# Optimization experiments

Measured on AMD Instinct MI355X. Metric: run time of the kernel, lower is better.

## Reference

```python
import jax, jax.numpy as jnp
import numpy as np

B, T, D = 2, 2048, 2048
H, KV, HD = 32, 8, 64
N_REP = H // KV
THETA = 10000.0
NEG_INF = -1e30


def _rope_tables(seq_len, head_dim, theta):
    inv_freq = 1.0 / (theta ** (jnp.arange(0, head_dim, 2, dtype=jnp.float32) / head_dim))
    t = jnp.arange(seq_len, dtype=jnp.float32)
    freqs = jnp.outer(t, inv_freq)                 # (T, HD/2)
    emb = jnp.concatenate([freqs, freqs], axis=-1)  # (T, HD)
    return jnp.cos(emb), jnp.sin(emb)


def _rotate_half(x):
    half = x.shape[-1] // 2
    return jnp.concatenate([-x[..., half:], x[..., :half]], axis=-1)


def setup_inputs() -> dict:
    key = jax.random.key(0)
    ks = jax.random.split(key, 5)
    s = 0.02  # keep logits in a sane range
    x = jax.random.normal(ks[0], (B, T, D), dtype=jnp.float32)
    Wq = jax.random.normal(ks[1], (D, H * HD), dtype=jnp.float32) * s
    Wk = jax.random.normal(ks[2], (D, KV * HD), dtype=jnp.float32) * s
    Wv = jax.random.normal(ks[3], (D, KV * HD), dtype=jnp.float32) * s
    Wo = jax.random.normal(ks[4], (D, D), dtype=jnp.float32) * s
    cos, sin = _rope_tables(T, HD, THETA)  # start_pos=0 since past_kv is None
    return {"x": x, "Wq": Wq, "Wk": Wk, "Wv": Wv, "Wo": Wo, "cos": cos, "sin": sin}


def reference(x, Wq, Wk, Wv, Wo, cos, sin):
    b, t, _ = x.shape
    # projections -> (B, heads, T, HD)
    q = (x @ Wq).reshape(b, t, H, HD).transpose(0, 2, 1, 3)
    k = (x @ Wk).reshape(b, t, KV, HD).transpose(0, 2, 1, 3)
    v = (x @ Wv).reshape(b, t, KV, HD).transpose(0, 2, 1, 3)
    # RoPE (cos/sin broadcast over batch and heads)
    c = cos[None, None, :, :]
    s = sin[None, None, :, :]
    q = q * c + _rotate_half(q) * s
    k = k * c + _rotate_half(k) * s
    # GQA: broadcast KV heads instead of repeat_interleave.
    # repeat_interleave(n_rep, dim=1) maps query head h -> kv head h // n_rep,
    # which equals reshape H -> (KV, N_REP).
    qg = q.reshape(b, KV, N_REP, t, HD)
    scale = 1.0 / jnp.sqrt(jnp.float32(HD))
    scores = jnp.einsum('bgrtd,bgsd->bgrts', qg, k) * scale  # (B,KV,N_REP,T,T)
    causal = jnp.tril(jnp.ones((t, t), dtype=bool))
    scores = jnp.where(causal[None, None, None, :, :], scores, NEG_INF)
    probs = jax.nn.softmax(scores, axis=-1)
    y = jnp.einsum('bgrts,bgsd->bgrtd', probs, v)            # (B,KV,N_REP,T,HD)
    y = y.reshape(b, H, t, HD).transpose(0, 2, 1, 3).reshape(b, t, H * HD)
    return y @ Wo
```

## Files before the change

kernel.cpp:

```cpp
#include <hip/hip_runtime.h>
#include <hip/hip_bf16.h>

constexpr int Bc  = 2;
constexpr int Tc  = 2048;
constexpr int Dc  = 2048;
constexpr int Hc  = 32;
constexpr int KVc = 8;
constexpr int HDc = 64;
constexpr int Mrows = Bc * Tc;
constexpr int QKVW  = 3072;
constexpr float SCALE = 0.125f;

typedef __attribute__((ext_vector_type(8))) short  bf16x8;
typedef __attribute__((ext_vector_type(4))) short  short4v;
typedef __attribute__((ext_vector_type(4))) float  f32x4;

__device__ __forceinline__ short f2bf(float f) {
    unsigned u = __builtin_bit_cast(unsigned, f);
    unsigned r = (u + 0x7FFFu + ((u >> 16) & 1u)) >> 16;
    return (short)(unsigned short)r;
}

__device__ __forceinline__ void load_lds16(const void* g, void* l) {
    __builtin_amdgcn_global_load_lds(
        (const __attribute__((address_space(1))) unsigned int*)g,
        (__attribute__((address_space(3))) unsigned int*)l,
        16, 0, 0);
}

__global__ void conv_bf16(const float* __restrict__ in, short* __restrict__ out, int n) {
    int i = (blockIdx.x * blockDim.x + threadIdx.x) * 8;
    if (i >= n) return;
    f32x4 a = *(const f32x4*)(in + i);
    f32x4 b = *(const f32x4*)(in + i + 4);
    bf16x8 o;
    o[0] = f2bf(a[0]); o[1] = f2bf(a[1]); o[2] = f2bf(a[2]); o[3] = f2bf(a[3]);
    o[4] = f2bf(b[0]); o[5] = f2bf(b[1]); o[6] = f2bf(b[2]); o[7] = f2bf(b[3]);
    *(bf16x8*)(out + i) = o;
}

__global__ __launch_bounds__(256) void transpose_conv(const float* __restrict__ in,
                                                      short* __restrict__ out,
                                                      int N, int ldo, int n0r) {
    __shared__ float T[64][68];
    const int k0 = blockIdx.y * 64;
    const int n0 = blockIdx.x * 64;
    const int t  = threadIdx.x;
    const int c4 = (t & 15) * 4;
    const int rr = t >> 4;
#pragma unroll
    for (int r = 0; r < 4; ++r) {
        int k = rr + 16 * r;
        float4 v = *(const float4*)(in + (size_t)(k0 + k) * N + n0 + c4);
        *(float4*)&T[k][c4] = v;
    }
    __syncthreads();
#pragma unroll
    for (int r = 0; r < 4; ++r) {
        int n = rr + 16 * r;
        short4v s;
        s[0] = f2bf(T[c4 + 0][n]); s[1] = f2bf(T[c4 + 1][n]);
        s[2] = f2bf(T[c4 + 2][n]); s[3] = f2bf(T[c4 + 3][n]);
        *(short4v*)(out + (size_t)(n0r + n0 + n) * ldo + k0 + c4) = s;
    }
}

__global__ __launch_bounds__(256) void gemm_mfma(const short* __restrict__ A,
                                                 const short* __restrict__ Bt,
                                                 float* __restrict__ C,
                                                 int M, int N, int K) {
    __shared__ short Al[128 * 64];
    __shared__ short Bl[128 * 64];
    const int tid = threadIdx.x;
    const int l  = tid & 63;
    const int w  = tid >> 6;
    const int lr = l & 15;
    const int lg = l >> 4;
    const int wm = w >> 1, wn = w & 1;

    const int nwg = gridDim.x * gridDim.y;
    const int bid0 = blockIdx.y * gridDim.x + blockIdx.x;
    const int cpx = nwg >> 3;
    const int swz = (bid0 & 7) * cpx + (bid0 >> 3);
    const int bm = (swz / gridDim.x) * 128;
    const int bn = (swz % gridDim.x) * 128;

    f32x4 acc[4][4];
#pragma unroll
    for (int i = 0; i < 4; ++i)
#pragma unroll
        for (int j = 0; j < 4; ++j) acc[i][j] = f32x4{0.f, 0.f, 0.f, 0.f};

    const int srow_off = l >> 3;
    const int sunit    = l & 7;

    for (int k0 = 0; k0 < K; k0 += 64) {
        __syncthreads();
#pragma unroll
        for (int j = 0; j < 4; ++j) {
            const int q   = w + 4 * j;
            const int row = 8 * q + srow_off;
            const int ug  = sunit ^ (row & 7);
            load_lds16(A  + (size_t)(bm + row) * K + k0 + ug * 8, (short*)Al + 512 * q);
            load_lds16(Bt + (size_t)(bn + row) * K + k0 + ug * 8, (short*)Bl + 512 * q);
        }
        __syncthreads();

#pragma unroll
        for (int ks = 0; ks < 2; ++ks) {
            bf16x8 af[4], bf[4];
#pragma unroll
            for (int mb = 0; mb < 4; ++mb) {
                const int row = wm * 64 + mb * 16 + lr;
                const int u   = (ks * 4 + lg) ^ (row & 7);
                af[mb] = *(const bf16x8*)(Al + row * 64 + u * 8);
            }
#pragma unroll
            for (int nb = 0; nb < 4; ++nb) {
                const int row = wn * 64 + nb * 16 + lr;
                const int u   = (ks * 4 + lg) ^ (row & 7);
                bf[nb] = *(const bf16x8*)(Bl + row * 64 + u * 8);
            }
#pragma unroll
            for (int mb = 0; mb < 4; ++mb)
#pragma unroll
                for (int nb = 0; nb < 4; ++nb)
                    acc[mb][nb] = __builtin_amdgcn_mfma_f32_16x16x32_bf16(
                        af[mb], bf[nb], acc[mb][nb], 0, 0, 0);
        }
    }

#pragma unroll
    for (int mb = 0; mb < 4; ++mb)
#pragma unroll
        for (int r = 0; r < 4; ++r) {
            const int row = bm + wm * 64 + mb * 16 + lg * 4 + r;
            float* cp = C + (size_t)row * N + bn + wn * 64 + lr;
#pragma unroll
            for (int nb = 0; nb < 4; ++nb) cp[nb * 16] = acc[mb][nb][r];
        }
}

__global__ void rope_pack_qk(const float* __restrict__ qkv,
                             const float* __restrict__ cosT,
                             const float* __restrict__ sinT,
                             short* __restrict__ qb, short* __restrict__ kb,
                             int total) {
    int idx = blockIdx.x * blockDim.x + threadIdx.x;
    if (idx >= total) return;
    int d   = idx & 31;
    int hh  = (idx >> 5) % 40;
    int row = idx / (32 * 40);
    int t   = row & (Tc - 1);
    int b   = row >> 11;
    float c = cosT[t * HDc + d];
    float s = sinT[t * HDc + d];
    if (hh < 32) {
        const float* p = qkv + (size_t)row * QKVW + hh * 64;
        float x0 = p[d], x1 = p[d + 32];
        short* qp = qb + (((size_t)(b * Hc + hh) * Tc + t) * 64);
        qp[d]      = f2bf((x0 * c - x1 * s) * SCALE);
        qp[d + 32] = f2bf((x1 * c + x0 * s) * SCALE);
    } else {
        int g = hh - 32;
        const float* p = qkv + (size_t)row * QKVW + 2048 + g * 64;
        float x0 = p[d], x1 = p[d + 32];
        short* kp = kb + (((size_t)(b * KVc + g) * Tc + t) * 64);
        kp[d]      = f2bf(x0 * c - x1 * s);
        kp[d + 32] = f2bf(x1 * c + x0 * s);
    }
}

__global__ __launch_bounds__(256) void pack_vt(const float* __restrict__ qkv,
                                               short* __restrict__ vtb) {
    __shared__ float T[64][68];
    const int t0 = blockIdx.x * 64;
    const int g  = blockIdx.y;
    const int b  = blockIdx.z;
    const int tt = threadIdx.x;
    const int c4 = (tt & 15) * 4;
    const int rr = tt >> 4;
    const float* src = qkv + 2560 + g * 64;
#pragma unroll
    for (int r = 0; r < 4; ++r) {
        int t = rr + 16 * r;
        float4 v = *(const float4*)(src + (size_t)(b * Tc + t0 + t) * QKVW + c4);
        *(float4*)&T[t][c4] = v;
    }
    __syncthreads();
    short* dst = vtb + ((size_t)(b * KVc + g) * 64) * Tc;
#pragma unroll
    for (int r = 0; r < 4; ++r) {
        int d = rr + 16 * r;
        short4v s;
        s[0] = f2bf(T[c4 + 0][d]); s[1] = f2bf(T[c4 + 1][d]);
        s[2] = f2bf(T[c4 + 2][d]); s[3] = f2bf(T[c4 + 3][d]);
        *(short4v*)(dst + (size_t)d * Tc + t0 + c4) = s;
    }
}

__global__ __launch_bounds__(64) void attn_gqa(const short* __restrict__ qb,
                                               const short* __restrict__ kb,
                                               const short* __restrict__ vtb,
                                               short* __restrict__ yb) {
    __shared__ short Ps[16][72];
    const int l  = threadIdx.x;
    const int lr = l & 15;
    const int lg = l >> 4;
    const int h  = blockIdx.y;
    const int b  = blockIdx.z;
    const int g  = h >> 2;

    const short* qhb = qb  + ((size_t)(b * Hc  + h) * Tc) * 64;
    const short* khb = kb  + ((size_t)(b * KVc + g) * Tc) * 64;
    const short* vhb = vtb + ((size_t)(b * KVc + g) * 64) * Tc;

#pragma unroll
    for (int half = 0; half < 2; ++half) {
        const int j   = half ? (127 - (int)blockIdx.x) : (int)blockIdx.x;
        const int qt0 = j * 16;

        bf16x8 qf0 = *(const bf16x8*)(qhb + (size_t)(qt0 + lr) * 64 + lg * 8);
        bf16x8 qf1 = *(const bf16x8*)(qhb + (size_t)(qt0 + lr) * 64 + 32 + lg * 8);

        f32x4 o[4];
#pragma unroll
        for (int i = 0; i < 4; ++i) o[i] = f32x4{0.f, 0.f, 0.f, 0.f};
        float mr[4], ls[4];
#pragma unroll
        for (int i = 0; i < 4; ++i) { mr[i] = -1e30f; ls[i] = 0.f; }

        const int nsteps = (qt0 >> 6) + 1;
        for (int st = 0; st < nsteps; ++st) {
            const int kv0 = st * 64;

            f32x4 c[4];
#pragma unroll
            for (int kbk = 0; kbk < 4; ++kbk) {
                const short* kr = khb + (size_t)(kv0 + 16 * kbk + lr) * 64;
                bf16x8 k0 = *(const bf16x8*)(kr + lg * 8);
                bf16x8 k1 = *(const bf16x8*)(kr + 32 + lg * 8);
                f32x4 acc = f32x4{0.f, 0.f, 0.f, 0.f};
                acc = __builtin_amdgcn_mfma_f32_16x16x32_bf16(qf0, k0, acc, 0, 0, 0);
                acc = __builtin_amdgcn_mfma_f32_16x16x32_bf16(qf1, k1, acc, 0, 0, 0);
                c[kbk] = acc;
            }

            if (st == nsteps - 1) {
#pragma unroll
                for (int kbk = 0; kbk < 4; ++kbk)
#pragma unroll
                    for (int r = 0; r < 4; ++r)
                        if (kv0 + lr + 16 * kbk > qt0 + lg * 4 + r) c[kbk][r] = -1e30f;
            }

#pragma unroll
            for (int r = 0; r < 4; ++r) {
                float tm = fmaxf(fmaxf(c[0][r], c[1][r]), fmaxf(c[2][r], c[3][r]));
                tm = fmaxf(tm, __shfl_xor(tm, 1));
                tm = fmaxf(tm, __shfl_xor(tm, 2));
                tm = fmaxf(tm, __shfl_xor(tm, 4));
                tm = fmaxf(tm, __shfl_xor(tm, 8));
                if (tm > mr[r]) {
                    const float corr = __expf(mr[r] - tm);
                    mr[r] = tm;
                    ls[r] *= corr;
#pragma unroll
                    for (int db = 0; db < 4; ++db) o[db][r] *= corr;
                }
                float rs = 0.f;
#pragma unroll
                for (int kbk = 0; kbk < 4; ++kbk) {
                    float p = __expf(c[kbk][r] - mr[r]);
                    c[kbk][r] = p;
                    rs += p;
                }
                rs += __shfl_xor(rs, 1);
                rs += __shfl_xor(rs, 2);
                rs += __shfl_xor(rs, 4);
                rs += __shfl_xor(rs, 8);
                ls[r] += rs;
#pragma unroll
                for (int kbk = 0; kbk < 4; ++kbk)
                    Ps[lg * 4 + r][lr + 16 * kbk] = f2bf(c[kbk][r]);
            }

#pragma unroll
            for (int ks = 0; ks < 2; ++ks) {
                bf16x8 pa = *(const bf16x8*)&Ps[lr][lg * 8 + ks * 32];
#pragma unroll
                for (int db = 0; db < 4; ++db) {
                    bf16x8 vv = *(const bf16x8*)(vhb + (size_t)(db * 16 + lr) * Tc
                                                 + kv0 + ks * 32 + lg * 8);
                    o[db] = __builtin_amdgcn_mfma_f32_16x16x32_bf16(pa, vv, o[db], 0, 0, 0);
                }
            }
        }

#pragma unroll
        for (int r = 0; r < 4; ++r) {
            const float inv = 1.0f / ls[r];
            short* yp = yb + (size_t)(b * Tc + qt0 + lg * 4 + r) * Dc + h * 64;
#pragma unroll
            for (int db = 0; db < 4; ++db)
                yp[lr + 16 * db] = f2bf(o[db][r] * inv);
        }
    }
}

extern "C" void kernel_launch(void* const* d_in, const int* in_sizes, int n_in,
                              void* d_out, int out_size, void* d_ws, size_t ws_size,
                              hipStream_t stream) {
    const float* x    = (const float*)d_in[0];
    const float* Wq   = (const float*)d_in[1];
    const float* Wk   = (const float*)d_in[2];
    const float* Wv   = (const float*)d_in[3];
    const float* Wo   = (const float*)d_in[4];
    const float* cosT = (const float*)d_in[5];
    const float* sinT = (const float*)d_in[6];
    float* out = (float*)d_out;

    short* xb    = (short*)d_ws;
    short* Wqkvt = xb + (size_t)Mrows * Dc;
    short* Wot   = Wqkvt + (size_t)QKVW * Dc;
    short* ybuf  = Wot + (size_t)Dc * Dc;
    float* qkv   = (float*)(ybuf + (size_t)Mrows * Dc);
    short* qbp = xb;
    short* kbp = Wqkvt;
    short* vtb = Wqkvt + (size_t)Bc * KVc * Tc * 64;

    conv_bf16<<<(Mrows * Dc / 8 + 255) / 256, 256, 0, stream>>>(x, xb, Mrows * Dc);
    transpose_conv<<<dim3(Dc / 64, Dc / 64), 256, 0, stream>>>(Wq, Wqkvt, Dc, Dc, 0);
    transpose_conv<<<dim3(512 / 64, Dc / 64), 256, 0, stream>>>(Wk, Wqkvt, 512, Dc, 2048);
    transpose_conv<<<dim3(512 / 64, Dc / 64), 256, 0, stream>>>(Wv, Wqkvt, 512, Dc, 2560);
    transpose_conv<<<dim3(Dc / 64, Dc / 64), 256, 0, stream>>>(Wo, Wot, Dc, Dc, 0);

    gemm_mfma<<<dim3(QKVW / 128, Mrows / 128), 256, 0, stream>>>(xb, Wqkvt, qkv, Mrows, QKVW, Dc);

    {
        int total = Mrows * (Hc + KVc) * 32;
        rope_pack_qk<<<(total + 255) / 256, 256, 0, stream>>>(qkv, cosT, sinT, qbp, kbp, total);
        pack_vt<<<dim3(Tc / 64, KVc, Bc), 256, 0, stream>>>(qkv, vtb);
    }

    attn_gqa<<<dim3(64, Hc, Bc), 64, 0, stream>>>(qbp, kbp, vtb, ybuf);

    gemm_mfma<<<dim3(Dc / 128, Mrows / 128), 256, 0, stream>>>(ybuf, Wot, out, Mrows, Dc, Dc);
}
```

Measured before the change: 525.3 us.

## Pack four query tiles per attention block and double-buffer K/V register prefetch

The attention kernel now runs four 64-lane waves per block, each owning one consecutive 16-row query tile, instead of one wave handling a balanced pair of tiles. K fragments for the next KV step are prefetched into a second register set, and V fragments are loaded at the start of each step, so global load latency overlaps the QK MFMAs and softmax. This raises register pressure and drops the front/back causal tile pairing, which may worsen load balance across blocks.

```diff
diff --git a/kernel.cpp b/kernel.cpp
--- a/kernel.cpp
+++ b/kernel.cpp
@@ -199,112 +199,138 @@
     }
 }
 
-__global__ __launch_bounds__(64) void attn_gqa(const short* __restrict__ qb,
-                                               const short* __restrict__ kb,
-                                               const short* __restrict__ vtb,
-                                               short* __restrict__ yb) {
-    __shared__ short Ps[16][72];
-    const int l  = threadIdx.x;
+__global__ __launch_bounds__(256, 3) void attn_gqa(const short* __restrict__ qb,
+                                                   const short* __restrict__ kb,
+                                                   const short* __restrict__ vtb,
+                                                   short* __restrict__ yb) {
+    __shared__ short Ps[4][16][72];
+    const int tid = threadIdx.x;
+    const int l  = tid & 63;
+    const int w  = tid >> 6;
     const int lr = l & 15;
     const int lg = l >> 4;
+    const int j  = (blockIdx.x << 2) | w;
     const int h  = blockIdx.y;
     const int b  = blockIdx.z;
     const int g  = h >> 2;
+    const int qt0 = j * 16;
 
     const short* qhb = qb  + ((size_t)(b * Hc  + h) * Tc) * 64;
     const short* khb = kb  + ((size_t)(b * KVc + g) * Tc) * 64;
     const short* vhb = vtb + ((size_t)(b * KVc + g) * 64) * Tc;
 
-#pragma unroll
-    for (int half = 0; half < 2; ++half) {
-        const int j   = half ? (127 - (int)blockIdx.x) : (int)blockIdx.x;
-        const int qt0 = j * 16;
-
-        bf16x8 qf0 = *(const bf16x8*)(qhb + (size_t)(qt0 + lr) * 64 + lg * 8);
-        bf16x8 qf1 = *(const bf16x8*)(qhb + (size_t)(qt0 + lr) * 64 + 32 + lg * 8);
-
-        f32x4 o[4];
-#pragma unroll
-        for (int i = 0; i < 4; ++i) o[i] = f32x4{0.f, 0.f, 0.f, 0.f};
-        float mr[4], ls[4];
-#pragma unroll
-        for (int i = 0; i < 4; ++i) { mr[i] = -1e30f; ls[i] = 0.f; }
-
-        const int nsteps = (qt0 >> 6) + 1;
-        for (int st = 0; st < nsteps; ++st) {
-            const int kv0 = st * 64;
-
-            f32x4 c[4];
+    const bf16x8 qf0 = *(const bf16x8*)(qhb + (size_t)(qt0 + lr) * 64 + lg * 8);
+    const bf16x8 qf1 = *(const bf16x8*)(qhb + (size_t)(qt0 + lr) * 64 + 32 + lg * 8);
+
+    f32x4 o[4];
+#pragma unroll
+    for (int i = 0; i < 4; ++i) o[i] = f32x4{0.f, 0.f, 0.f, 0.f};
+    float mr[4], ls[4];
+#pragma unroll
+    for (int i = 0; i < 4; ++i) { mr[i] = -1e30f; ls[i] = 0.f; }
+
+    const int nsteps = (qt0 >> 6) + 1;
+
+    bf16x8 kfa[8], kfb[8];
+
+#pragma unroll
+    for (int kbk = 0; kbk < 4; ++kbk) {
+        const short* kr = khb + (size_t)(16 * kbk + lr) * 64;
+        kfa[2 * kbk]     = *(const bf16x8*)(kr + lg * 8);
+        kfa[2 * kbk + 1] = *(const bf16x8*)(kr + 32 + lg * 8);
+    }
+
+    auto step = [&](int st, bf16x8 (&kcur)[8], bf16x8 (&knxt)[8]) {
+        const int kv0 = st * 64;
+
+        bf16x8 vv[8];
+#pragma unroll
+        for (int ks = 0; ks < 2; ++ks)
+#pragma unroll
+            for (int db = 0; db < 4; ++db)
+                vv[ks * 4 + db] = *(const bf16x8*)(vhb + (size_t)(db * 16 + lr) * Tc
+                                                   + kv0 + ks * 32 + lg * 8);
+
+        f32x4 c[4];
+#pragma unroll
+        for (int kbk = 0; kbk < 4; ++kbk) {
+            f32x4 acc = f32x4{0.f, 0.f, 0.f, 0.f};
+            acc = __builtin_amdgcn_mfma_f32_16x16x32_bf16(qf0, kcur[2 * kbk],     acc, 0, 0, 0);
+            acc = __builtin_amdgcn_mfma_f32_16x16x32_bf16(qf1, kcur[2 * kbk + 1], acc, 0, 0, 0);
+            c[kbk] = acc;
+        }
+
+        if (st + 1 < nsteps) {
+            const int kn = kv0 + 64;
 #pragma unroll
             for (int kbk = 0; kbk < 4; ++kbk) {
-                const short* kr = khb + (size_t)(kv0 + 16 * kbk + lr) * 64;
-                bf16x8 k0 = *(const bf16x8*)(kr + lg * 8);
-                bf16x8 k1 = *(const bf16x8*)(kr + 32 + lg * 8);
-                f32x4 acc = f32x4{0.f, 0.f, 0.f, 0.f};
-                acc = __builtin_amdgcn_mfma_f32_16x16x32_bf16(qf0, k0, acc, 0, 0, 0);
-                acc = __builtin_amdgcn_mfma_f32_16x16x32_bf16(qf1, k1, acc, 0, 0, 0);
-                c[kbk] = acc;
-            }
-
-            if (st == nsteps - 1) {
-#pragma unroll
-                for (int kbk = 0; kbk < 4; ++kbk)
-#pragma unroll
-                    for (int r = 0; r < 4; ++r)
-                        if (kv0 + lr + 16 * kbk > qt0 + lg * 4 + r) c[kbk][r] = -1e30f;
-            }
-
-#pragma unroll
-            for (int r = 0; r < 4; ++r) {
-                float tm = fmaxf(fmaxf(c[0][r], c[1][r]), fmaxf(c[2][r], c[3][r]));
-                tm = fmaxf(tm, __shfl_xor(tm, 1));
-                tm = fmaxf(tm, __shfl_xor(tm, 2));
-                tm = fmaxf(tm, __shfl_xor(tm, 4));
-                tm = fmaxf(tm, __shfl_xor(tm, 8));
-                if (tm > mr[r]) {
-                    const float corr = __expf(mr[r] - tm);
-                    mr[r] = tm;
-                    ls[r] *= corr;
-#pragma unroll
-                    for (int db = 0; db < 4; ++db) o[db][r] *= corr;
-                }
-                float rs = 0.f;
-#pragma unroll
-                for (int kbk = 0; kbk < 4; ++kbk) {
-                    float p = __expf(c[kbk][r] - mr[r]);
-                    c[kbk][r] = p;
-                    rs += p;
-                }
-                rs += __shfl_xor(rs, 1);
-                rs += __shfl_xor(rs, 2);
-                rs += __shfl_xor(rs, 4);
-                rs += __shfl_xor(rs, 8);
-                ls[r] += rs;
-#pragma unroll
-                for (int kbk = 0; kbk < 4; ++kbk)
-                    Ps[lg * 4 + r][lr + 16 * kbk] = f2bf(c[kbk][r]);
-            }
-
-#pragma unroll
-            for (int ks = 0; ks < 2; ++ks) {
-                bf16x8 pa = *(const bf16x8*)&Ps[lr][lg * 8 + ks * 32];
-#pragma unroll
-                for (int db = 0; db < 4; ++db) {
-                    bf16x8 vv = *(const bf16x8*)(vhb + (size_t)(db * 16 + lr) * Tc
-                                                 + kv0 + ks * 32 + lg * 8);
-                    o[db] = __builtin_amdgcn_mfma_f32_16x16x32_bf16(pa, vv, o[db], 0, 0, 0);
-                }
-            }
+                const short* kr = khb + (size_t)(kn + 16 * kbk + lr) * 64;
+                knxt[2 * kbk]     = *(const bf16x8*)(kr + lg * 8);
+                knxt[2 * kbk + 1] = *(const bf16x8*)(kr + 32 + lg * 8);
+            }
+        }
+
+        if (st == nsteps - 1) {
+#pragma unroll
+            for (int kbk = 0; kbk < 4; ++kbk)
+#pragma unroll
+                for (int r = 0; r < 4; ++r)
+                    if (kv0 + lr + 16 * kbk > qt0 + lg * 4 + r) c[kbk][r] = -1e30f;
         }
 
 #pragma unroll
         for (int r = 0; r < 4; ++r) {
-            const float inv = 1.0f / ls[r];
-            short* yp = yb + (size_t)(b * Tc + qt0 + lg * 4 + r) * Dc + h * 64;
+            float tm = fmaxf(fmaxf(c[0][r], c[1][r]), fmaxf(c[2][r], c[3][r]));
+            tm = fmaxf(tm, __shfl_xor(tm, 1));
+            tm = fmaxf(tm, __shfl_xor(tm, 2));
+            tm = fmaxf(tm, __shfl_xor(tm, 4));
+            tm = fmaxf(tm, __shfl_xor(tm, 8));
+            if (tm > mr[r]) {
+                const float corr = __expf(mr[r] - tm);
+                mr[r] = tm;
+                ls[r] *= corr;
+#pragma unroll
+                for (int db = 0; db < 4; ++db) o[db][r] *= corr;
+            }
+            float rs = 0.f;
+#pragma unroll
+            for (int kbk = 0; kbk < 4; ++kbk) {
+                float p = __expf(c[kbk][r] - mr[r]);
+                c[kbk][r] = p;
+                rs += p;
+            }
+            rs += __shfl_xor(rs, 1);
+            rs += __shfl_xor(rs, 2);
+            rs += __shfl_xor(rs, 4);
+            rs += __shfl_xor(rs, 8);
+            ls[r] += rs;
+#pragma unroll
+            for (int kbk = 0; kbk < 4; ++kbk)
+                Ps[w][lg * 4 + r][lr + 16 * kbk] = f2bf(c[kbk][r]);
+        }
+
+#pragma unroll
+        for (int ks = 0; ks < 2; ++ks) {
+            bf16x8 pa = *(const bf16x8*)&Ps[w][lr][lg * 8 + ks * 32];
 #pragma unroll
             for (int db = 0; db < 4; ++db)
-                yp[lr + 16 * db] = f2bf(o[db][r] * inv);
-        }
+                o[db] = __builtin_amdgcn_mfma_f32_16x16x32_bf16(pa, vv[ks * 4 + db],
+                                                                o[db], 0, 0, 0);
+        }
+    };
+
+    for (int st = 0; st < nsteps; st += 2) {
+        step(st, kfa, kfb);
+        if (st + 1 < nsteps) step(st + 1, kfb, kfa);
+    }
+
+#pragma unroll
+    for (int r = 0; r < 4; ++r) {
+        const float inv = 1.0f / ls[r];
+        short* yp = yb + (size_t)(b * Tc + qt0 + lg * 4 + r) * Dc + h * 64;
+#pragma unroll
+        for (int db = 0; db < 4; ++db)
+            yp[lr + 16 * db] = f2bf(o[db][r] * inv);
     }
 }
 
@@ -343,7 +369,7 @@
         pack_vt<<<dim3(Tc / 64, KVc, Bc), 256, 0, stream>>>(qkv, vtb);
     }
 
-    attn_gqa<<<dim3(64, Hc, Bc), 64, 0, stream>>>(qbp, kbp, vtb, ybuf);
+    attn_gqa<<<dim3(32, Hc, Bc), 256, 0, stream>>>(qbp, kbp, vtb, ybuf);
 
     gemm_mfma<<<dim3(Dc / 128, Mrows / 128), 256, 0, stream>>>(ybuf, Wot, out, Mrows, Dc, Dc);
 }
```

Measured after the change: 757.7 us. +44.2%, slower.

## Process two 16-row query tiles per wave, four waves per attention block

Applied to the files above, without the earlier changes.

The attention kernel now gives each wave a 32-row query tile (two 16-row sub-tiles) and reuses each loaded K fragment and V fragment for both sub-tiles, halving global K/V loads per query row. Blocks grow from one wave to four, with the tiles mixed so that each block's causal work is balanced, and the grid shrinks accordingly. Each wave keeps a private LDS probability buffer guarded by wave-level barriers. In exchange, register pressure rises and the causal mask covers coarser 32-row tiles, so a few extra fully masked key entries get processed.

```diff
diff --git a/kernel.cpp b/kernel.cpp
--- a/kernel.cpp
+++ b/kernel.cpp
@@ -26,6 +26,12 @@
         (const __attribute__((address_space(1))) unsigned int*)g,
         (__attribute__((address_space(3))) unsigned int*)l,
         16, 0, 0);
+}
+
+__device__ __forceinline__ void lds_fence() {
+    __builtin_amdgcn_sched_barrier(0);
+    __builtin_amdgcn_wave_barrier();
+    __builtin_amdgcn_sched_barrier(0);
 }
 
 __global__ void conv_bf16(const float* __restrict__ in, short* __restrict__ out, int n) {
@@ -199,111 +205,145 @@
     }
 }
 
-__global__ __launch_bounds__(64) void attn_gqa(const short* __restrict__ qb,
-                                               const short* __restrict__ kb,
-                                               const short* __restrict__ vtb,
-                                               short* __restrict__ yb) {
-    __shared__ short Ps[16][72];
-    const int l  = threadIdx.x;
+__global__ __launch_bounds__(256, 2) void attn_gqa(const short* __restrict__ qb,
+                                                   const short* __restrict__ kb,
+                                                   const short* __restrict__ vtb,
+                                                   short* __restrict__ yb) {
+    __shared__ short Ps[4][2][16][72];
+    const int tid = threadIdx.x;
+    const int l  = tid & 63;
+    const int w  = tid >> 6;
     const int lr = l & 15;
     const int lg = l >> 4;
+    const int bx = blockIdx.x;
+    const int a  = (w & 2) ? ((w & 1) ? 63 - bx : 32 + bx)
+                           : ((w & 1) ? 31 - bx : bx);
     const int h  = blockIdx.y;
     const int b  = blockIdx.z;
     const int g  = h >> 2;
+    const int qA = a * 32;
 
     const short* qhb = qb  + ((size_t)(b * Hc  + h) * Tc) * 64;
     const short* khb = kb  + ((size_t)(b * KVc + g) * Tc) * 64;
     const short* vhb = vtb + ((size_t)(b * KVc + g) * 64) * Tc;
 
-#pragma unroll
-    for (int half = 0; half < 2; ++half) {
-        const int j   = half ? (127 - (int)blockIdx.x) : (int)blockIdx.x;
-        const int qt0 = j * 16;
-
-        bf16x8 qf0 = *(const bf16x8*)(qhb + (size_t)(qt0 + lr) * 64 + lg * 8);
-        bf16x8 qf1 = *(const bf16x8*)(qhb + (size_t)(qt0 + lr) * 64 + 32 + lg * 8);
-
-        f32x4 o[4];
-#pragma unroll
-        for (int i = 0; i < 4; ++i) o[i] = f32x4{0.f, 0.f, 0.f, 0.f};
-        float mr[4], ls[4];
-#pragma unroll
-        for (int i = 0; i < 4; ++i) { mr[i] = -1e30f; ls[i] = 0.f; }
-
-        const int nsteps = (qt0 >> 6) + 1;
-        for (int st = 0; st < nsteps; ++st) {
-            const int kv0 = st * 64;
-
-            f32x4 c[4];
+    const bf16x8 qA0 = *(const bf16x8*)(qhb + (size_t)(qA + lr) * 64 + lg * 8);
+    const bf16x8 qA1 = *(const bf16x8*)(qhb + (size_t)(qA + lr) * 64 + 32 + lg * 8);
+    const bf16x8 qB0 = *(const bf16x8*)(qhb + (size_t)(qA + 16 + lr) * 64 + lg * 8);
+    const bf16x8 qB1 = *(const bf16x8*)(qhb + (size_t)(qA + 16 + lr) * 64 + 32 + lg * 8);
+
+    f32x4 oA[4], oB[4];
+#pragma unroll
+    for (int i = 0; i < 4; ++i) { oA[i] = f32x4{0.f,0.f,0.f,0.f}; oB[i] = f32x4{0.f,0.f,0.f,0.f}; }
+    float mA[4], lA[4], mB[4], lB[4];
+#pragma unroll
+    for (int i = 0; i < 4; ++i) { mA[i] = -1e30f; lA[i] = 0.f; mB[i] = -1e30f; lB[i] = 0.f; }
+
+    const int nsteps = ((qA + 31) >> 6) + 1;
+
+    for (int st = 0; st < nsteps; ++st) {
+        const int kv0 = st * 64;
+
+        bf16x8 kf[8];
+#pragma unroll
+        for (int kbk = 0; kbk < 4; ++kbk) {
+            const short* kr = khb + (size_t)(kv0 + 16 * kbk + lr) * 64;
+            kf[2 * kbk]     = *(const bf16x8*)(kr + lg * 8);
+            kf[2 * kbk + 1] = *(const bf16x8*)(kr + 32 + lg * 8);
+        }
+
+        f32x4 cA[4], cB[4];
+#pragma unroll
+        for (int kbk = 0; kbk < 4; ++kbk) {
+            f32x4 acc = f32x4{0.f,0.f,0.f,0.f};
+            acc = __builtin_amdgcn_mfma_f32_16x16x32_bf16(qA0, kf[2*kbk],   acc, 0, 0, 0);
+            acc = __builtin_amdgcn_mfma_f32_16x16x32_bf16(qA1, kf[2*kbk+1], acc, 0, 0, 0);
+            cA[kbk] = acc;
+            f32x4 acb = f32x4{0.f,0.f,0.f,0.f};
+            acb = __builtin_amdgcn_mfma_f32_16x16x32_bf16(qB0, kf[2*kbk],   acb, 0, 0, 0);
+            acb = __builtin_amdgcn_mfma_f32_16x16x32_bf16(qB1, kf[2*kbk+1], acb, 0, 0, 0);
+            cB[kbk] = acb;
+        }
+
+        if (st == nsteps - 1) {
+#pragma unroll
+            for (int kbk = 0; kbk < 4; ++kbk)
+#pragma unroll
+                for (int r = 0; r < 4; ++r) {
+                    const int key = kv0 + lr + 16 * kbk;
+                    if (key > qA + lg * 4 + r)      cA[kbk][r] = -1e30f;
+                    if (key > qA + 16 + lg * 4 + r) cB[kbk][r] = -1e30f;
+                }
+        }
+
+#pragma unroll
+        for (int r = 0; r < 4; ++r) {
+            float tA = fmaxf(fmaxf(cA[0][r], cA[1][r]), fmaxf(cA[2][r], cA[3][r]));
+            float tB = fmaxf(fmaxf(cB[0][r], cB[1][r]), fmaxf(cB[2][r], cB[3][r]));
+            tA = fmaxf(tA, __shfl_xor(tA, 1));  tB = fmaxf(tB, __shfl_xor(tB, 1));
+            tA = fmaxf(tA, __shfl_xor(tA, 2));  tB = fmaxf(tB, __shfl_xor(tB, 2));
+            tA = fmaxf(tA, __shfl_xor(tA, 4));  tB = fmaxf(tB, __shfl_xor(tB, 4));
+            tA = fmaxf(tA, __shfl_xor(tA, 8));  tB = fmaxf(tB, __shfl_xor(tB, 8));
+            if (tA > mA[r]) {
+                const float corr = __expf(mA[r] - tA);
+                mA[r] = tA; lA[r] *= corr;
+#pragma unroll
+                for (int db = 0; db < 4; ++db) oA[db][r] *= corr;
+            }
+            if (tB > mB[r]) {
+                const float corr = __expf(mB[r] - tB);
+                mB[r] = tB; lB[r] *= corr;
+#pragma unroll
+                for (int db = 0; db < 4; ++db) oB[db][r] *= corr;
+            }
+            float rA = 0.f, rB = 0.f;
 #pragma unroll
             for (int kbk = 0; kbk < 4; ++kbk) {
-                const short* kr = khb + (size_t)(kv0 + 16 * kbk + lr) * 64;
-                bf16x8 k0 = *(const bf16x8*)(kr + lg * 8);
-                bf16x8 k1 = *(const bf16x8*)(kr + 32 + lg * 8);
-                f32x4 acc = f32x4{0.f, 0.f, 0.f, 0.f};
-                acc = __builtin_amdgcn_mfma_f32_16x16x32_bf16(qf0, k0, acc, 0, 0, 0);
-                acc = __builtin_amdgcn_mfma_f32_16x16x32_bf16(qf1, k1, acc, 0, 0, 0);
-                c[kbk] = acc;
-            }
-
-            if (st == nsteps - 1) {
-#pragma unroll
-                for (int kbk = 0; kbk < 4; ++kbk)
-#pragma unroll
-                    for (int r = 0; r < 4; ++r)
-                        if (kv0 + lr + 16 * kbk > qt0 + lg * 4 + r) c[kbk][r] = -1e30f;
-            }
-
-#pragma unroll
-            for (int r = 0; r < 4; ++r) {
-                float tm = fmaxf(fmaxf(c[0][r], c[1][r]), fmaxf(c[2][r], c[3][r]));
-                tm = fmaxf(tm, __shfl_xor(tm, 1));
-                tm = fmaxf(tm, __shfl_xor(tm, 2));
-                tm = fmaxf(tm, __shfl_xor(tm, 4));
-                tm = fmaxf(tm, __shfl_xor(tm, 8));
-                if (tm > mr[r]) {
-                    const float corr = __expf(mr[r] - tm);
-                    mr[r] = tm;
-                    ls[r] *= corr;
-#pragma unroll
-                    for (int db = 0; db < 4; ++db) o[db][r] *= corr;
-                }
-                float rs = 0.f;
-#pragma unroll
-                for (int kbk = 0; kbk < 4; ++kbk) {
-                    float p = __expf(c[kbk][r] - mr[r]);
-                    c[kbk][r] = p;
-                    rs += p;
-                }
-                rs += __shfl_xor(rs, 1);
-                rs += __shfl_xor(rs, 2);
-                rs += __shfl_xor(rs, 4);
-                rs += __shfl_xor(rs, 8);
-                ls[r] += rs;
-#pragma unroll
-                for (int kbk = 0; kbk < 4; ++kbk)
-                    Ps[lg * 4 + r][lr + 16 * kbk] = f2bf(c[kbk][r]);
-            }
-
-#pragma unroll
-            for (int ks = 0; ks < 2; ++ks) {
-                bf16x8 pa = *(const bf16x8*)&Ps[lr][lg * 8 + ks * 32];
-#pragma unroll
-                for (int db = 0; db < 4; ++db) {
-                    bf16x8 vv = *(const bf16x8*)(vhb + (size_t)(db * 16 + lr) * Tc
-                                                 + kv0 + ks * 32 + lg * 8);
-                    o[db] = __builtin_amdgcn_mfma_f32_16x16x32_bf16(pa, vv, o[db], 0, 0, 0);
-                }
-            }
-        }
-
-#pragma unroll
-        for (int r = 0; r < 4; ++r) {
-            const float inv = 1.0f / ls[r];
-            short* yp = yb + (size_t)(b * Tc + qt0 + lg * 4 + r) * Dc + h * 64;
-#pragma unroll
-            for (int db = 0; db < 4; ++db)
-                yp[lr + 16 * db] = f2bf(o[db][r] * inv);
+                float pA = __expf(cA[kbk][r] - mA[r]);
+                float pB = __expf(cB[kbk][r] - mB[r]);
+                cA[kbk][r] = pA; rA += pA;
+                cB[kbk][r] = pB; rB += pB;
+            }
+            rA += __shfl_xor(rA, 1);  rB += __shfl_xor(rB, 1);
+            rA += __shfl_xor(rA, 2);  rB += __shfl_xor(rB, 2);
+            rA += __shfl_xor(rA, 4);  rB += __shfl_xor(rB, 4);
+            rA += __shfl_xor(rA, 8);  rB += __shfl_xor(rB, 8);
+            lA[r] += rA;  lB[r] += rB;
+#pragma unroll
+            for (int kbk = 0; kbk < 4; ++kbk) {
+                Ps[w][0][lg * 4 + r][lr + 16 * kbk] = f2bf(cA[kbk][r]);
+                Ps[w][1][lg * 4 + r][lr + 16 * kbk] = f2bf(cB[kbk][r]);
+            }
+        }
+
+        lds_fence();
+
+#pragma unroll
+        for (int ks = 0; ks < 2; ++ks) {
+            bf16x8 paA = *(const bf16x8*)&Ps[w][0][lr][lg * 8 + ks * 32];
+            bf16x8 paB = *(const bf16x8*)&Ps[w][1][lr][lg * 8 + ks * 32];
+#pragma unroll
+            for (int db = 0; db < 4; ++db) {
+                bf16x8 vv = *(const bf16x8*)(vhb + (size_t)(db * 16 + lr) * Tc
+                                             + kv0 + ks * 32 + lg * 8);
+                oA[db] = __builtin_amdgcn_mfma_f32_16x16x32_bf16(paA, vv, oA[db], 0, 0, 0);
+                oB[db] = __builtin_amdgcn_mfma_f32_16x16x32_bf16(paB, vv, oB[db], 0, 0, 0);
+            }
+        }
+
+        lds_fence();
+    }
+
+#pragma unroll
+    for (int r = 0; r < 4; ++r) {
+        const float iA = 1.0f / lA[r];
+        const float iB = 1.0f / lB[r];
+        short* ypA = yb + (size_t)(b * Tc + qA + lg * 4 + r) * Dc + h * 64;
+        short* ypB = yb + (size_t)(b * Tc + qA + 16 + lg * 4 + r) * Dc + h * 64;
+#pragma unroll
+        for (int db = 0; db < 4; ++db) {
+            ypA[lr + 16 * db] = f2bf(oA[db][r] * iA);
+            ypB[lr + 16 * db] = f2bf(oB[db][r] * iB);
         }
     }
 }
@@ -343,7 +383,7 @@
         pack_vt<<<dim3(Tc / 64, KVc, Bc), 256, 0, stream>>>(qkv, vtb);
     }
 
-    attn_gqa<<<dim3(64, Hc, Bc), 64, 0, stream>>>(qbp, kbp, vtb, ybuf);
+    attn_gqa<<<dim3(16, Hc, Bc), 256, 0, stream>>>(qbp, kbp, vtb, ybuf);
 
     gemm_mfma<<<dim3(Dc / 128, Mrows / 128), 256, 0, stream>>>(ybuf, Wot, out, Mrows, Dc, Dc);
 }
```

Result: faster. 470.8 us (-10.4%).
